# Kernel tuning notes

Measured on AMD Instinct MI355X. Metric: run time of the kernel, lower is better.

## Reference

```python
import jax, jax.numpy as jnp
import numpy as np

D_MODEL = 1024
D_STATE = 16
D_CONV = 4
EXPAND = 2
N_LAYERS = 4
D_INNER = EXPAND * D_MODEL          # 2048
DT_RANK = (D_MODEL + 15) // 16     # 64
BATCH, SEQ = 2, 1024
LN_EPS = 1e-5


def setup_inputs() -> dict:
    key = jax.random.key(0)
    ks = jax.random.split(key, 10)
    s = 0.02
    A_log = jnp.log(jnp.broadcast_to(
        jnp.arange(1, D_STATE + 1, dtype=jnp.float32), (N_LAYERS, D_INNER, D_STATE)))
    return {
        "x": jax.random.normal(ks[0], (BATCH, SEQ, D_MODEL), jnp.float32),
        "in_proj_w": jax.random.normal(ks[1], (N_LAYERS, 2 * D_INNER, D_MODEL), jnp.float32) * s,
        "conv_w": jax.random.normal(ks[2], (N_LAYERS, D_INNER, D_CONV), jnp.float32) * s,
        "conv_b": jnp.zeros((N_LAYERS, D_INNER), jnp.float32),
        "x_proj_w": jax.random.normal(ks[3], (N_LAYERS, DT_RANK + 2 * D_STATE, D_INNER), jnp.float32) * s,
        "dt_proj_w": jax.random.normal(ks[4], (N_LAYERS, D_INNER, DT_RANK), jnp.float32) * s,
        "dt_proj_b": jax.random.uniform(ks[5], (N_LAYERS, D_INNER), jnp.float32, -5.0, -3.0),
        "A_log": A_log,
        "D_skip": jnp.ones((N_LAYERS, D_INNER), jnp.float32),
        "out_proj_w": jax.random.normal(ks[6], (N_LAYERS, D_MODEL, D_INNER), jnp.float32) * s,
        "ln_g": jnp.ones((D_MODEL,), jnp.float32),
        "ln_b": jnp.zeros((D_MODEL,), jnp.float32),
    }


def _layer_norm(x, g, b):
    mu = jnp.mean(x, axis=-1, keepdims=True)
    var = jnp.mean(jnp.square(x - mu), axis=-1, keepdims=True)
    return (x - mu) * jax.lax.rsqrt(var + LN_EPS) * g + b


def _scan_combine(e1, e2):
    a1, b1 = e1
    a2, b2 = e2
    return a1 * a2, a2 * b1 + b2


def _mamba_block(x, in_w, cw, cb, xp_w, dt_w, dt_b, A_log, D_skip, out_w):
    # x: [B, L, D]
    xz = jnp.einsum('bld,ed->ble', x, in_w)          # [B, L, 2*d_inner]
    xm, z = jnp.split(xz, 2, axis=-1)
    # causal depthwise conv over time
    xc = jnp.transpose(xm, (0, 2, 1))                 # [B, d_inner, L]
    xc = jax.lax.conv_general_dilated(
        xc, cw[:, None, :], window_strides=(1,), padding=[(D_CONV - 1, 0)],
        feature_group_count=D_INNER, dimension_numbers=('NCH', 'OIH', 'NCH'))
    xm = jax.nn.silu(jnp.transpose(xc, (0, 2, 1)) + cb[None, None, :])
    # input-dependent dt, B, C
    xdbl = jnp.einsum('bld,ed->ble', xm, xp_w)        # [B, L, dt_rank + 2*S]
    dt, Bm, Cm = jnp.split(xdbl, [DT_RANK, DT_RANK + D_STATE], axis=-1)
    dt = jax.nn.softplus(jnp.einsum('blr,dr->bld', dt, dt_w) + dt_b)   # [B, L, d_inner]
    A = -jnp.exp(A_log)                               # [d_inner, S]
    dA = jnp.exp(dt[..., None] * A)                   # [B, L, d_inner, S]
    dBu = dt[..., None] * Bm[:, :, None, :] * xm[..., None]
    # selective scan: h_t = dA_t * h_{t-1} + dBu_t, via associative scan over L
    _, h = jax.lax.associative_scan(_scan_combine, (dA, dBu), axis=1)
    y = jnp.einsum('blds,bls->bld', h, Cm) + xm * D_skip
    y = y * jax.nn.silu(z)
    return jnp.einsum('bld,od->blo', y, out_w)        # [B, L, D]


def reference(x, in_proj_w, conv_w, conv_b, x_proj_w, dt_proj_w, dt_proj_b,
              A_log, D_skip, out_proj_w, ln_g, ln_b):
    for i in range(N_LAYERS):
        x = x + _mamba_block(_layer_norm(x, ln_g, ln_b),
                             in_proj_w[i], conv_w[i], conv_b[i], x_proj_w[i],
                             dt_proj_w[i], dt_proj_b[i], A_log[i], D_skip[i],
                             out_proj_w[i])
    return _layer_norm(x, ln_g, ln_b)
```

## Files before the change

kernel.cpp:

```cpp
#include <hip/hip_runtime.h>

#define NTOK 2048
#define SEQL 1024
#define DMODEL 1024
#define DINNER 2048
#define DSTATE 16
#define DTRANK 64
#define GCH 64
#define LC 16
#define XDS 128
#define XSPK 8

typedef __attribute__((ext_vector_type(8))) short short8;
typedef __attribute__((ext_vector_type(4))) float float4v;

__device__ __forceinline__ unsigned short f2bf(float f) {
    unsigned u = __float_as_uint(f);
    unsigned r = u + 0x7FFFu + ((u >> 16) & 1u);
    return (unsigned short)(r >> 16);
}
__device__ __forceinline__ float bf2f(unsigned short h) {
    return __uint_as_float(((unsigned)h) << 16);
}

__global__ __launch_bounds__(256) void f32_to_bf16_4(
    const float* __restrict__ s0, unsigned short* __restrict__ d0, int c0,
    const float* __restrict__ s1, unsigned short* __restrict__ d1, int c1,
    const float* __restrict__ s2, unsigned short* __restrict__ d2, int c2,
    const float* __restrict__ s3, unsigned short* __restrict__ d3, int c3) {
    int i = blockIdx.x * 256 + threadIdx.x;
    if (i >= c3) return;
    const float* s; unsigned short* dd; int j;
    if (i < c0)      { s = s0; dd = d0; j = i; }
    else if (i < c1) { s = s1; dd = d1; j = i - c0; }
    else if (i < c2) { s = s2; dd = d2; j = i - c1; }
    else             { s = s3; dd = d3; j = i - c2; }
    float4 a = ((const float4*)s)[4 * j];
    float4 b = ((const float4*)s)[4 * j + 1];
    float4 c = ((const float4*)s)[4 * j + 2];
    float4 d = ((const float4*)s)[4 * j + 3];
    uint4 v0, v1;
    v0.x = (unsigned)f2bf(a.x) | ((unsigned)f2bf(a.y) << 16);
    v0.y = (unsigned)f2bf(a.z) | ((unsigned)f2bf(a.w) << 16);
    v0.z = (unsigned)f2bf(b.x) | ((unsigned)f2bf(b.y) << 16);
    v0.w = (unsigned)f2bf(b.z) | ((unsigned)f2bf(b.w) << 16);
    v1.x = (unsigned)f2bf(c.x) | ((unsigned)f2bf(c.y) << 16);
    v1.y = (unsigned)f2bf(c.z) | ((unsigned)f2bf(c.w) << 16);
    v1.z = (unsigned)f2bf(d.x) | ((unsigned)f2bf(d.y) << 16);
    v1.w = (unsigned)f2bf(d.z) | ((unsigned)f2bf(d.w) << 16);
    ((uint4*)dd)[2 * j]     = v0;
    ((uint4*)dd)[2 * j + 1] = v1;
}

__global__ __launch_bounds__(256) void ln_kernel(
    const float* __restrict__ x, float* __restrict__ x_copy,
    const float* __restrict__ g, const float* __restrict__ b,
    unsigned short* __restrict__ out_bf) {
    int row = blockIdx.x;
    int t = threadIdx.x;
    float4 v = ((const float4*)(x + (size_t)row * DMODEL))[t];
    ((float4*)(x_copy + (size_t)row * DMODEL))[t] = v;
    float s  = v.x + v.y + v.z + v.w;
    float ss = v.x*v.x + v.y*v.y + v.z*v.z + v.w*v.w;
    for (int o = 32; o; o >>= 1) { s += __shfl_xor(s, o); ss += __shfl_xor(ss, o); }
    __shared__ float red[8];
    int wv = t >> 6;
    if ((t & 63) == 0) { red[wv * 2] = s; red[wv * 2 + 1] = ss; }
    __syncthreads();
    s  = red[0] + red[2] + red[4] + red[6];
    ss = red[1] + red[3] + red[5] + red[7];
    float mu = s * (1.f / DMODEL);
    float rstd = rsqrtf(ss * (1.f / DMODEL) - mu * mu + 1e-5f);
    float4 gv = ((const float4*)g)[t];
    float4 bv = ((const float4*)b)[t];
    ((ushort4*)out_bf)[row * 256 + t] = make_ushort4(
        f2bf((v.x - mu) * rstd * gv.x + bv.x),
        f2bf((v.y - mu) * rstd * gv.y + bv.y),
        f2bf((v.z - mu) * rstd * gv.z + bv.z),
        f2bf((v.w - mu) * rstd * gv.w + bv.w));
}

__global__ __launch_bounds__(256) void residual_ln(
    float* __restrict__ x_res, const float* __restrict__ p0,
    const float* __restrict__ p1, const float* __restrict__ p2,
    const float* __restrict__ p3, const float* __restrict__ g,
    const float* __restrict__ b, unsigned short* __restrict__ out_bf,
    float* __restrict__ out_f32) {
    int row = blockIdx.x;
    int t = threadIdx.x;
    size_t o4 = (size_t)row * 256 + t;
    float4 v  = ((const float4*)x_res)[o4];
    float4 a0 = ((const float4*)p0)[o4];
    float4 a1 = ((const float4*)p1)[o4];
    float4 a2 = ((const float4*)p2)[o4];
    float4 a3 = ((const float4*)p3)[o4];
    v.x += (a0.x + a1.x) + (a2.x + a3.x);
    v.y += (a0.y + a1.y) + (a2.y + a3.y);
    v.z += (a0.z + a1.z) + (a2.z + a3.z);
    v.w += (a0.w + a1.w) + (a2.w + a3.w);
    ((float4*)x_res)[o4] = v;
    float s  = v.x + v.y + v.z + v.w;
    float ss = v.x*v.x + v.y*v.y + v.z*v.z + v.w*v.w;
    for (int o = 32; o; o >>= 1) { s += __shfl_xor(s, o); ss += __shfl_xor(ss, o); }
    __shared__ float red[8];
    int wv = t >> 6;
    if ((t & 63) == 0) { red[wv * 2] = s; red[wv * 2 + 1] = ss; }
    __syncthreads();
    s  = red[0] + red[2] + red[4] + red[6];
    ss = red[1] + red[3] + red[5] + red[7];
    float mu = s * (1.f / DMODEL);
    float rstd = rsqrtf(ss * (1.f / DMODEL) - mu * mu + 1e-5f);
    float4 gv = ((const float4*)g)[t];
    float4 bv = ((const float4*)b)[t];
    float o0 = (v.x - mu) * rstd * gv.x + bv.x;
    float o1 = (v.y - mu) * rstd * gv.y + bv.y;
    float o2 = (v.z - mu) * rstd * gv.z + bv.z;
    float o3 = (v.w - mu) * rstd * gv.w + bv.w;
    if (out_f32) {
        ((float4*)out_f32)[o4] = make_float4(o0, o1, o2, o3);
    } else {
        ((ushort4*)out_bf)[o4] = make_ushort4(f2bf(o0), f2bf(o1), f2bf(o2), f2bf(o3));
    }
}

#define BKG 32
__global__ __launch_bounds__(256) void gemm64(
    const unsigned short* __restrict__ A, const unsigned short* __restrict__ B,
    void* __restrict__ Cv, const float* __restrict__ bias,
    int M, int N, int K, int Nb, int mode) {
    __shared__ __attribute__((aligned(16))) unsigned short As[3][128 * BKG];
    __shared__ __attribute__((aligned(16))) unsigned short Bs[3][64 * BKG];
    int m0 = blockIdx.y * 128, n0 = blockIdx.x * 64;
    int Klocal = K / gridDim.z;
    int kstart = blockIdx.z * Klocal;
    int t = threadIdx.x;
    int lane = t & 63, w = t >> 6;
    int tr = lane & 15, quad = lane >> 4;
    int r_l = lane >> 2;
    int q_l = (lane & 3) ^ ((lane >> 3) & 3);
    int col_l = q_l * 8;

    float4v acc[2][4];
    for (int mi = 0; mi < 2; ++mi)
        for (int ni = 0; ni < 4; ++ni)
            acc[mi][ni] = (float4v){0.f, 0.f, 0.f, 0.f};

    auto stage = [&](int kt, int buf) {
        int kbase = kstart + kt * BKG;
#pragma unroll
        for (int j = 0; j < 2; ++j) {
            int c = w * 2 + j;
            const unsigned short* ga = A + (size_t)(m0 + c * 16 + r_l) * K + kbase + col_l;
            __builtin_amdgcn_global_load_lds(
                (const __attribute__((address_space(1))) void*)ga,
                (__attribute__((address_space(3))) void*)(&As[buf][c * 512]),
                16, 0, 0);
        }
        int brow = n0 + w * 16 + r_l;
        if (brow >= Nb) brow = Nb - 1;
        const unsigned short* gb = B + (size_t)brow * K + kbase + col_l;
        __builtin_amdgcn_global_load_lds(
            (const __attribute__((address_space(1))) void*)gb,
            (__attribute__((address_space(3))) void*)(&Bs[buf][w * 512]),
            16, 0, 0);
    };

    int KT = Klocal / BKG;
    stage(0, 0);
    if (KT > 1) stage(1, 1);
    int u_off = (tr * 4 + (quad ^ ((tr >> 1) & 3))) * 8;
    for (int kt = 0; kt < KT; ++kt) {
        int cur = kt % 3;
        if (kt + 2 < KT) stage(kt + 2, (kt + 2) % 3);
        asm volatile("" ::: "memory");
        int nleft = KT - kt - 1;
        if (nleft >= 2)      __builtin_amdgcn_s_waitcnt(0x0F76);
        else if (nleft == 1) __builtin_amdgcn_s_waitcnt(0x0F73);
        else                 __builtin_amdgcn_s_waitcnt(0x0F70);
        __builtin_amdgcn_s_barrier();
        asm volatile("" ::: "memory");
        short8 af[2], bfr[4];
#pragma unroll
        for (int i = 0; i < 2; ++i)
            af[i] = *(const short8*)(&As[cur][(w * 2 + i) * 512 + u_off]);
#pragma unroll
        for (int i = 0; i < 4; ++i)
            bfr[i] = *(const short8*)(&Bs[cur][i * 512 + u_off]);
#pragma unroll
        for (int mi = 0; mi < 2; ++mi)
#pragma unroll
            for (int ni = 0; ni < 4; ++ni)
                acc[mi][ni] = __builtin_amdgcn_mfma_f32_16x16x32_bf16(
                    af[mi], bfr[ni], acc[mi][ni], 0, 0, 0);
        asm volatile("" ::: "memory");
        __builtin_amdgcn_s_barrier();
        asm volatile("" ::: "memory");
    }
    size_t zoff = (size_t)blockIdx.z * M * N;
    for (int mi = 0; mi < 2; ++mi)
        for (int ni = 0; ni < 4; ++ni) {
            int col = n0 + ni * 16 + tr;
            int rowb = m0 + w * 32 + mi * 16 + quad * 4;
            for (int r = 0; r < 4; ++r) {
                size_t off = (size_t)(rowb + r) * N + col;
                float val = acc[mi][ni][r];
                if (mode == 0) {
                    ((float*)Cv)[zoff + off] = val;
                } else if (mode == 2) {
                    ((unsigned short*)Cv)[off] = f2bf(val);
                } else {
                    float v2 = val + bias[col];
                    float sp = (v2 > 15.f) ? v2 : log1pf(expf(v2));
                    ((unsigned short*)Cv)[off] = f2bf(sp);
                }
            }
        }
}

__global__ __launch_bounds__(256) void reduce_xp(
    const float* __restrict__ part, unsigned short* __restrict__ dtA,
    float* __restrict__ BC) {
    int i = blockIdx.x * 256 + threadIdx.x;
    int row = i >> 7, col = i & 127;
    float s = 0.f;
#pragma unroll
    for (int z = 0; z < XSPK; ++z)
        s += part[(size_t)z * NTOK * XDS + i];
    if (col < 64) dtA[row * 64 + col] = f2bf(s);
    else if (col < 96) BC[row * 32 + (col - 64)] = s;
}

__global__ __launch_bounds__(256) void conv_silu(
    const unsigned short* __restrict__ xz, const float* __restrict__ cw,
    const float* __restrict__ cb, unsigned short* __restrict__ xm_bf) {
    int i = blockIdx.x * 256 + threadIdx.x;
    int c8 = i & (DINNER / 8 - 1);
    int tk = i >> 8;
    int l = tk & (SEQL - 1);
    int c = c8 * 8;
    const unsigned short* base = xz + (size_t)tk * (2 * DINNER) + c;
    short8 r3 = {0,0,0,0,0,0,0,0}, r2 = {0,0,0,0,0,0,0,0}, r1 = {0,0,0,0,0,0,0,0};
    if (l >= 3) r3 = *(const short8*)(base - 3 * 2 * DINNER);
    if (l >= 2) r2 = *(const short8*)(base - 2 * 2 * DINNER);
    if (l >= 1) r1 = *(const short8*)(base - 1 * 2 * DINNER);
    short8 r0 = *(const short8*)(base);
    short8 out;
#pragma unroll
    for (int j = 0; j < 8; ++j) {
        float4 wv = ((const float4*)cw)[c + j];
        float acc = cb[c + j]
            + bf2f((unsigned short)r3[j]) * wv.x
            + bf2f((unsigned short)r2[j]) * wv.y
            + bf2f((unsigned short)r1[j]) * wv.z
            + bf2f((unsigned short)r0[j]) * wv.w;
        float sv = acc / (1.f + expf(-acc));
        out[j] = (short)f2bf(sv);
    }
    *(short8*)(xm_bf + (size_t)tk * DINNER + c) = out;
}

__global__ __launch_bounds__(256) void scan_a(
    const unsigned short* __restrict__ dt_bf, const unsigned short* __restrict__ xm_bf,
    const float* __restrict__ BC, const float* __restrict__ A_log,
    float* __restrict__ h_end, float* __restrict__ S_chunk) {
    int bid = blockIdx.x;
    int g = bid >> 4, b = (bid >> 3) & 1, cbk = bid & 7;
    int c = cbk * 256 + threadIdx.x;
    __shared__ float Bsh[LC][16];
    {
        int li = threadIdx.x >> 4, s = threadIdx.x & 15;
        Bsh[li][s] = BC[((size_t)(b * SEQL + g * LC + li)) * 32 + s];
    }
    __syncthreads();
    float a_l2[16], h[16];
#pragma unroll
    for (int s = 0; s < 16; ++s) {
        a_l2[s] = -expf(A_log[c * 16 + s]) * 1.44269504f;
        h[s] = 0.f;
    }
    float S = 0.f;
    int rowbase = b * SEQL + g * LC;
    for (int i = 0; i < LC; ++i) {
        size_t off = (size_t)(rowbase + i) * DINNER + c;
        float dtv = bf2f(dt_bf[off]);
        S += dtv;
        float u = bf2f(xm_bf[off]);
        float bu = dtv * u;
#pragma unroll
        for (int s = 0; s < 16; ++s) {
            float dA = exp2f(dtv * a_l2[s]);
            h[s] = dA * h[s] + Bsh[i][s] * bu;
        }
    }
    int gb = g * 2 + b;
#pragma unroll
    for (int s = 0; s < 16; ++s)
        h_end[((size_t)gb * 16 + s) * DINNER + c] = h[s];
    S_chunk[(size_t)gb * DINNER + c] = S;
}

__global__ __launch_bounds__(256) void scan_b(
    const float* __restrict__ A_log, const float* __restrict__ S_chunk,
    const float* __restrict__ h_end, float* __restrict__ h_in) {
    int idx = blockIdx.x * 256 + threadIdx.x;
    int c = idx & (DINNER - 1);
    int s = (idx >> 11) & 15;
    int b = idx >> 15;
    float a_l2 = -expf(A_log[c * 16 + s]) * 1.44269504f;
    float h = 0.f;
    for (int g = 0; g < GCH; ++g) {
        int gb = g * 2 + b;
        h_in[((size_t)gb * 16 + s) * DINNER + c] = h;
        float P = exp2f(a_l2 * S_chunk[(size_t)gb * DINNER + c]);
        h = P * h + h_end[((size_t)gb * 16 + s) * DINNER + c];
    }
}

__global__ __launch_bounds__(256) void scan_c(
    const unsigned short* __restrict__ dt_bf, const unsigned short* __restrict__ xm_bf,
    const float* __restrict__ BC, const float* __restrict__ A_log,
    const float* __restrict__ D_skip, const unsigned short* __restrict__ xz,
    const float* __restrict__ h_in, unsigned short* __restrict__ y_bf) {
    int bid = blockIdx.x;
    int g = bid >> 4, b = (bid >> 3) & 1, cbk = bid & 7;
    int c = cbk * 256 + threadIdx.x;
    __shared__ float BCsh[LC][32];
    for (int r = 0; r < 2; ++r) {
        int e = threadIdx.x + r * 256;
        int li = e >> 5, s = e & 31;
        BCsh[li][s] = BC[((size_t)(b * SEQL + g * LC + li)) * 32 + s];
    }
    __syncthreads();
    int gb = g * 2 + b;
    float a_l2[16], h[16];
#pragma unroll
    for (int s = 0; s < 16; ++s) {
        a_l2[s] = -expf(A_log[c * 16 + s]) * 1.44269504f;
        h[s] = h_in[((size_t)gb * 16 + s) * DINNER + c];
    }
    float dsk = D_skip[c];
    int rowbase = b * SEQL + g * LC;
    for (int i = 0; i < LC; ++i) {
        size_t off = (size_t)(rowbase + i) * DINNER + c;
        float dtv = bf2f(dt_bf[off]);
        float u = bf2f(xm_bf[off]);
        float bu = dtv * u;
        float y = 0.f;
#pragma unroll
        for (int s = 0; s < 16; ++s) {
            float dA = exp2f(dtv * a_l2[s]);
            h[s] = dA * h[s] + BCsh[i][s] * bu;
            y += h[s] * BCsh[i][16 + s];
        }
        y += u * dsk;
        float zv = bf2f(xz[(size_t)(rowbase + i) * (2 * DINNER) + DINNER + c]);
        y *= zv / (1.f + expf(-zv));
        y_bf[off] = f2bf(y);
    }
}

extern "C" void kernel_launch(void* const* d_in, const int* in_sizes, int n_in,
                              void* d_out, int out_size, void* d_ws, size_t ws_size,
                              hipStream_t stream) {
    const float* x_in   = (const float*)d_in[0];
    const float* in_w   = (const float*)d_in[1];
    const float* conv_w = (const float*)d_in[2];
    const float* conv_b = (const float*)d_in[3];
    const float* xp_w   = (const float*)d_in[4];
    const float* dt_w   = (const float*)d_in[5];
    const float* dt_b   = (const float*)d_in[6];
    const float* A_logp = (const float*)d_in[7];
    const float* Dsk    = (const float*)d_in[8];
    const float* out_w  = (const float*)d_in[9];
    const float* ln_g   = (const float*)d_in[10];
    const float* ln_b   = (const float*)d_in[11];
    float* outp = (float*)d_out;

    char* p = (char*)d_ws;
    auto alloc = [&](size_t bytes) {
        void* r = (void*)p;
        p += (bytes + 255) & ~(size_t)255;
        return r;
    };
    float* x_res  = (float*)alloc((size_t)NTOK * DMODEL * 4);
    unsigned short* xn_bf = (unsigned short*)alloc((size_t)NTOK * DMODEL * 2);
    unsigned short* xz_bf = (unsigned short*)alloc((size_t)NTOK * 2 * DINNER * 2);
    unsigned short* xm_bf = (unsigned short*)alloc((size_t)NTOK * DINNER * 2);
    float* xp_part = (float*)alloc((size_t)XSPK * NTOK * XDS * 4);
    float* out_part = (float*)alloc((size_t)4 * NTOK * DMODEL * 4);
    float* BC     = (float*)alloc((size_t)NTOK * 32 * 4);
    unsigned short* dtA_bf = (unsigned short*)alloc((size_t)NTOK * DTRANK * 2);
    unsigned short* dt_bf = (unsigned short*)alloc((size_t)NTOK * DINNER * 2);
    unsigned short* y_bf = (unsigned short*)alloc((size_t)NTOK * DINNER * 2);
    float* h_end  = (float*)alloc((size_t)GCH * 2 * 16 * DINNER * 4);
    float* h_in   = (float*)alloc((size_t)GCH * 2 * 16 * DINNER * 4);
    float* S_chunk = (float*)alloc((size_t)GCH * 2 * DINNER * 4);
    int n_inw  = 4 * 2 * DINNER * DMODEL;
    int n_xpw  = 4 * 96 * DINNER;
    int n_dtw  = 4 * DINNER * DTRANK;
    int n_outw = 4 * DMODEL * DINNER;
    unsigned short* wbf_in  = (unsigned short*)alloc((size_t)n_inw * 2);
    unsigned short* wbf_xp  = (unsigned short*)alloc((size_t)n_xpw * 2);
    unsigned short* wbf_dt  = (unsigned short*)alloc((size_t)n_dtw * 2);
    unsigned short* wbf_out = (unsigned short*)alloc((size_t)n_outw * 2);

    int c0 = n_inw / 16;
    int c1 = c0 + n_xpw / 16;
    int c2 = c1 + n_dtw / 16;
    int c3 = c2 + n_outw / 16;
    f32_to_bf16_4<<<(c3 + 255) / 256, 256, 0, stream>>>(
        in_w, wbf_in, c0, xp_w, wbf_xp, c1, dt_w, wbf_dt, c2, out_w, wbf_out, c3);

    ln_kernel<<<NTOK, 256, 0, stream>>>(x_in, x_res, ln_g, ln_b, xn_bf);

    for (int L = 0; L < 4; ++L) {
        const unsigned short* w_in  = wbf_in  + (size_t)L * 2 * DINNER * DMODEL;
        const float*          w_cv  = conv_w  + (size_t)L * DINNER * 4;
        const float*          b_cv  = conv_b  + (size_t)L * DINNER;
        const unsigned short* w_xp  = wbf_xp  + (size_t)L * 96 * DINNER;
        const unsigned short* w_dt  = wbf_dt  + (size_t)L * DINNER * DTRANK;
        const float*          b_dt  = dt_b    + (size_t)L * DINNER;
        const float*          al    = A_logp  + (size_t)L * DINNER * DSTATE;
        const float*          dskl  = Dsk     + (size_t)L * DINNER;
        const unsigned short* w_out = wbf_out + (size_t)L * DMODEL * DINNER;

        gemm64<<<dim3(64, 16, 1), 256, 0, stream>>>(
            xn_bf, w_in, xz_bf, nullptr, NTOK, 2 * DINNER, DMODEL, 2 * DINNER, 2);
        conv_silu<<<NTOK * (DINNER / 8) / 256, 256, 0, stream>>>(xz_bf, w_cv, b_cv, xm_bf);
        gemm64<<<dim3(2, 16, XSPK), 256, 0, stream>>>(
            xm_bf, w_xp, xp_part, nullptr, NTOK, XDS, DINNER, 96, 0);
        reduce_xp<<<NTOK * XDS / 256, 256, 0, stream>>>(xp_part, dtA_bf, BC);
        gemm64<<<dim3(32, 16, 1), 256, 0, stream>>>(
            dtA_bf, w_dt, dt_bf, b_dt, NTOK, DINNER, DTRANK, DINNER, 3);
        scan_a<<<GCH * 16, 256, 0, stream>>>(dt_bf, xm_bf, BC, al, h_end, S_chunk);
        scan_b<<<2 * 16 * DINNER / 256, 256, 0, stream>>>(al, S_chunk, h_end, h_in);
        scan_c<<<GCH * 16, 256, 0, stream>>>(dt_bf, xm_bf, BC, al, dskl, xz_bf,
                                             h_in, y_bf);
        gemm64<<<dim3(16, 16, 4), 256, 0, stream>>>(
            y_bf, w_out, out_part, nullptr, NTOK, DMODEL, DINNER, DMODEL, 0);
        residual_ln<<<NTOK, 256, 0, stream>>>(
            x_res, out_part, out_part + (size_t)NTOK * DMODEL,
            out_part + (size_t)2 * NTOK * DMODEL, out_part + (size_t)3 * NTOK * DMODEL,
            ln_g, ln_b, (L < 3) ? xn_bf : nullptr, (L < 3) ? nullptr : outp);
    }
}
```

Before: 876.2 us.

## Fuse three scan kernels into one persistent kernel with grid barriers

Merges scan_a, scan_b and scan_c into a single kernel that uses a global atomic-counter grid barrier between the phases. Registers holding a_l2 and the shared BC tile are reused across phases, and two kernel launches plus their reloads are removed. The 1024-block grid must be fully co-resident (launch_bounds 256,4 on 256 CUs) or the barrier deadlocks. The counter is reset in the weight-conversion kernel and offset per layer.

```diff
diff --git a/kernel.cpp b/kernel.cpp
--- a/kernel.cpp
+++ b/kernel.cpp
@@ -23,12 +23,26 @@
     return __uint_as_float(((unsigned)h) << 16);
 }
 
+__device__ __forceinline__ void grid_bar(unsigned* cnt, unsigned target) {
+    __syncthreads();
+    if (threadIdx.x == 0) {
+        __threadfence();
+        atomicAdd(cnt, 1u);
+        while (__hip_atomic_load(cnt, __ATOMIC_ACQUIRE, __HIP_MEMORY_SCOPE_AGENT)
+               < target)
+            __builtin_amdgcn_s_sleep(8);
+    }
+    __syncthreads();
+}
+
 __global__ __launch_bounds__(256) void f32_to_bf16_4(
     const float* __restrict__ s0, unsigned short* __restrict__ d0, int c0,
     const float* __restrict__ s1, unsigned short* __restrict__ d1, int c1,
     const float* __restrict__ s2, unsigned short* __restrict__ d2, int c2,
-    const float* __restrict__ s3, unsigned short* __restrict__ d3, int c3) {
+    const float* __restrict__ s3, unsigned short* __restrict__ d3, int c3,
+    unsigned* __restrict__ bar) {
     int i = blockIdx.x * 256 + threadIdx.x;
+    if (i == 0) *bar = 0u;
     if (i >= c3) return;
     const float* s; unsigned short* dd; int j;
     if (i < c0)      { s = s0; dd = d0; j = i; }
@@ -259,17 +273,21 @@
     *(short8*)(xm_bf + (size_t)tk * DINNER + c) = out;
 }
 
-__global__ __launch_bounds__(256) void scan_a(
+__global__ __launch_bounds__(256, 4) void scan_fused(
     const unsigned short* __restrict__ dt_bf, const unsigned short* __restrict__ xm_bf,
     const float* __restrict__ BC, const float* __restrict__ A_log,
-    float* __restrict__ h_end, float* __restrict__ S_chunk) {
+    const float* __restrict__ D_skip, const unsigned short* __restrict__ xz,
+    float* __restrict__ h_end, float* __restrict__ S_chunk,
+    float* __restrict__ h_in, unsigned short* __restrict__ y_bf,
+    unsigned* __restrict__ bar, unsigned tbase) {
     int bid = blockIdx.x;
     int g = bid >> 4, b = (bid >> 3) & 1, cbk = bid & 7;
     int c = cbk * 256 + threadIdx.x;
-    __shared__ float Bsh[LC][16];
-    {
-        int li = threadIdx.x >> 4, s = threadIdx.x & 15;
-        Bsh[li][s] = BC[((size_t)(b * SEQL + g * LC + li)) * 32 + s];
+    __shared__ float BCsh[LC][32];
+    for (int r = 0; r < 2; ++r) {
+        int e = threadIdx.x + r * 256;
+        int li = e >> 5, s = e & 31;
+        BCsh[li][s] = BC[((size_t)(b * SEQL + g * LC + li)) * 32 + s];
     }
     __syncthreads();
     float a_l2[16], h[16];
@@ -289,7 +307,7 @@
 #pragma unroll
         for (int s = 0; s < 16; ++s) {
             float dA = exp2f(dtv * a_l2[s]);
-            h[s] = dA * h[s] + Bsh[i][s] * bu;
+            h[s] = dA * h[s] + BCsh[i][s] * bu;
         }
     }
     int gb = g * 2 + b;
@@ -297,49 +315,30 @@
     for (int s = 0; s < 16; ++s)
         h_end[((size_t)gb * 16 + s) * DINNER + c] = h[s];
     S_chunk[(size_t)gb * DINNER + c] = S;
-}
-
-__global__ __launch_bounds__(256) void scan_b(
-    const float* __restrict__ A_log, const float* __restrict__ S_chunk,
-    const float* __restrict__ h_end, float* __restrict__ h_in) {
-    int idx = blockIdx.x * 256 + threadIdx.x;
-    int c = idx & (DINNER - 1);
-    int s = (idx >> 11) & 15;
-    int b = idx >> 15;
-    float a_l2 = -expf(A_log[c * 16 + s]) * 1.44269504f;
-    float h = 0.f;
-    for (int g = 0; g < GCH; ++g) {
-        int gb = g * 2 + b;
-        h_in[((size_t)gb * 16 + s) * DINNER + c] = h;
-        float P = exp2f(a_l2 * S_chunk[(size_t)gb * DINNER + c]);
-        h = P * h + h_end[((size_t)gb * 16 + s) * DINNER + c];
-    }
-}
-
-__global__ __launch_bounds__(256) void scan_c(
-    const unsigned short* __restrict__ dt_bf, const unsigned short* __restrict__ xm_bf,
-    const float* __restrict__ BC, const float* __restrict__ A_log,
-    const float* __restrict__ D_skip, const unsigned short* __restrict__ xz,
-    const float* __restrict__ h_in, unsigned short* __restrict__ y_bf) {
-    int bid = blockIdx.x;
-    int g = bid >> 4, b = (bid >> 3) & 1, cbk = bid & 7;
-    int c = cbk * 256 + threadIdx.x;
-    __shared__ float BCsh[LC][32];
-    for (int r = 0; r < 2; ++r) {
-        int e = threadIdx.x + r * 256;
-        int li = e >> 5, s = e & 31;
-        BCsh[li][s] = BC[((size_t)(b * SEQL + g * LC + li)) * 32 + s];
-    }
-    __syncthreads();
-    int gb = g * 2 + b;
-    float a_l2[16], h[16];
-#pragma unroll
-    for (int s = 0; s < 16; ++s) {
-        a_l2[s] = -expf(A_log[c * 16 + s]) * 1.44269504f;
+
+    grid_bar(bar, tbase + 1024);
+
+    if (bid < 256) {
+        int idx = bid * 256 + threadIdx.x;
+        int cc = idx & (DINNER - 1);
+        int ss = (idx >> 11) & 15;
+        int bb = idx >> 15;
+        float al2 = -expf(A_log[cc * 16 + ss]) * 1.44269504f;
+        float hh = 0.f;
+        for (int gg = 0; gg < GCH; ++gg) {
+            int gb2 = gg * 2 + bb;
+            h_in[((size_t)gb2 * 16 + ss) * DINNER + cc] = hh;
+            float P = exp2f(al2 * S_chunk[(size_t)gb2 * DINNER + cc]);
+            hh = P * hh + h_end[((size_t)gb2 * 16 + ss) * DINNER + cc];
+        }
+    }
+
+    grid_bar(bar, tbase + 2048);
+
+#pragma unroll
+    for (int s = 0; s < 16; ++s)
         h[s] = h_in[((size_t)gb * 16 + s) * DINNER + c];
-    }
     float dsk = D_skip[c];
-    int rowbase = b * SEQL + g * LC;
     for (int i = 0; i < LC; ++i) {
         size_t off = (size_t)(rowbase + i) * DINNER + c;
         float dtv = bf2f(dt_bf[off]);
@@ -395,6 +394,7 @@
     float* h_end  = (float*)alloc((size_t)GCH * 2 * 16 * DINNER * 4);
     float* h_in   = (float*)alloc((size_t)GCH * 2 * 16 * DINNER * 4);
     float* S_chunk = (float*)alloc((size_t)GCH * 2 * DINNER * 4);
+    unsigned* bar = (unsigned*)alloc(256);
     int n_inw  = 4 * 2 * DINNER * DMODEL;
     int n_xpw  = 4 * 96 * DINNER;
     int n_dtw  = 4 * DINNER * DTRANK;
@@ -409,7 +409,7 @@
     int c2 = c1 + n_dtw / 16;
     int c3 = c2 + n_outw / 16;
     f32_to_bf16_4<<<(c3 + 255) / 256, 256, 0, stream>>>(
-        in_w, wbf_in, c0, xp_w, wbf_xp, c1, dt_w, wbf_dt, c2, out_w, wbf_out, c3);
+        in_w, wbf_in, c0, xp_w, wbf_xp, c1, dt_w, wbf_dt, c2, out_w, wbf_out, c3, bar);
 
     ln_kernel<<<NTOK, 256, 0, stream>>>(x_in, x_res, ln_g, ln_b, xn_bf);
 
@@ -432,10 +432,9 @@
         reduce_xp<<<NTOK * XDS / 256, 256, 0, stream>>>(xp_part, dtA_bf, BC);
         gemm64<<<dim3(32, 16, 1), 256, 0, stream>>>(
             dtA_bf, w_dt, dt_bf, b_dt, NTOK, DINNER, DTRANK, DINNER, 3);
-        scan_a<<<GCH * 16, 256, 0, stream>>>(dt_bf, xm_bf, BC, al, h_end, S_chunk);
-        scan_b<<<2 * 16 * DINNER / 256, 256, 0, stream>>>(al, S_chunk, h_end, h_in);
-        scan_c<<<GCH * 16, 256, 0, stream>>>(dt_bf, xm_bf, BC, al, dskl, xz_bf,
-                                             h_in, y_bf);
+        scan_fused<<<GCH * 16, 256, 0, stream>>>(
+            dt_bf, xm_bf, BC, al, dskl, xz_bf, h_end, S_chunk, h_in, y_bf,
+            bar, (unsigned)(L * 2048));
         gemm64<<<dim3(16, 16, 4), 256, 0, stream>>>(
             y_bf, w_out, out_part, nullptr, NTOK, DMODEL, DINNER, DMODEL, 0);
         residual_ln<<<NTOK, 256, 0, stream>>>(
```

After: 2.516 ms. 187% more time.

## Fuse dt projection and softplus into scan kernels, drop dt GEMM

Applied to the files above, without the earlier changes.

Removes the separate dt_proj GEMM and its bf16 dt buffer. Each scan kernel now recomputes dt per channel from the low-rank dtA vectors in shared memory and a transposed, pair-packed dt weight held in registers, then applies softplus inline. This avoids writing and reading a token-by-d_inner dt tensor and saves one launch per layer. In exchange the dt dot products are done twice (scan_a and scan_c) with scalar FMAs, and the kernels use 32 more registers each. A new kernel transposes the dt weights once at setup.

```diff
diff --git a/kernel.cpp b/kernel.cpp
--- a/kernel.cpp
+++ b/kernel.cpp
@@ -22,19 +22,19 @@
 __device__ __forceinline__ float bf2f(unsigned short h) {
     return __uint_as_float(((unsigned)h) << 16);
 }
-
-__global__ __launch_bounds__(256) void f32_to_bf16_4(
+__device__ __forceinline__ float bflo(unsigned u) { return __uint_as_float(u << 16); }
+__device__ __forceinline__ float bfhi(unsigned u) { return __uint_as_float(u & 0xffff0000u); }
+
+__global__ __launch_bounds__(256) void f32_to_bf16_3(
     const float* __restrict__ s0, unsigned short* __restrict__ d0, int c0,
     const float* __restrict__ s1, unsigned short* __restrict__ d1, int c1,
-    const float* __restrict__ s2, unsigned short* __restrict__ d2, int c2,
-    const float* __restrict__ s3, unsigned short* __restrict__ d3, int c3) {
+    const float* __restrict__ s2, unsigned short* __restrict__ d2, int c2) {
     int i = blockIdx.x * 256 + threadIdx.x;
-    if (i >= c3) return;
+    if (i >= c2) return;
     const float* s; unsigned short* dd; int j;
     if (i < c0)      { s = s0; dd = d0; j = i; }
     else if (i < c1) { s = s1; dd = d1; j = i - c0; }
-    else if (i < c2) { s = s2; dd = d2; j = i - c1; }
-    else             { s = s3; dd = d3; j = i - c2; }
+    else             { s = s2; dd = d2; j = i - c1; }
     float4 a = ((const float4*)s)[4 * j];
     float4 b = ((const float4*)s)[4 * j + 1];
     float4 c = ((const float4*)s)[4 * j + 2];
@@ -50,6 +50,17 @@
     v1.w = (unsigned)f2bf(d.z) | ((unsigned)f2bf(d.w) << 16);
     ((uint4*)dd)[2 * j]     = v0;
     ((uint4*)dd)[2 * j + 1] = v1;
+}
+
+__global__ __launch_bounds__(256) void cvt_dtT(
+    const float* __restrict__ w, unsigned short* __restrict__ wT) {
+    int idx = blockIdx.x * 256 + threadIdx.x;
+    int c = idx & (DINNER - 1);
+    int r = (idx >> 11) & 63;
+    int l = idx >> 17;
+    size_t lbase = (size_t)l * 64 * DINNER;
+    wT[lbase + ((size_t)(r >> 1) * DINNER + c) * 2 + (r & 1)] =
+        f2bf(w[(size_t)l * DINNER * 64 + (size_t)c * 64 + r]);
 }
 
 __global__ __launch_bounds__(256) void ln_kernel(
@@ -126,8 +137,7 @@
 #define BKG 32
 __global__ __launch_bounds__(256) void gemm64(
     const unsigned short* __restrict__ A, const unsigned short* __restrict__ B,
-    void* __restrict__ Cv, const float* __restrict__ bias,
-    int M, int N, int K, int Nb, int mode) {
+    void* __restrict__ Cv, int M, int N, int K, int Nb, int mode) {
     __shared__ __attribute__((aligned(16))) unsigned short As[3][128 * BKG];
     __shared__ __attribute__((aligned(16))) unsigned short Bs[3][64 * BKG];
     int m0 = blockIdx.y * 128, n0 = blockIdx.x * 64;
@@ -206,12 +216,8 @@
                 float val = acc[mi][ni][r];
                 if (mode == 0) {
                     ((float*)Cv)[zoff + off] = val;
-                } else if (mode == 2) {
+                } else {
                     ((unsigned short*)Cv)[off] = f2bf(val);
-                } else {
-                    float v2 = val + bias[col];
-                    float sp = (v2 > 15.f) ? v2 : log1pf(expf(v2));
-                    ((unsigned short*)Cv)[off] = f2bf(sp);
                 }
             }
         }
@@ -260,18 +266,28 @@
 }
 
 __global__ __launch_bounds__(256) void scan_a(
-    const unsigned short* __restrict__ dt_bf, const unsigned short* __restrict__ xm_bf,
+    const unsigned short* __restrict__ dtA, const unsigned short* __restrict__ wdtT,
+    const float* __restrict__ dtb, const unsigned short* __restrict__ xm_bf,
     const float* __restrict__ BC, const float* __restrict__ A_log,
     float* __restrict__ h_end, float* __restrict__ S_chunk) {
     int bid = blockIdx.x;
     int g = bid >> 4, b = (bid >> 3) & 1, cbk = bid & 7;
     int c = cbk * 256 + threadIdx.x;
+    int rowbase = b * SEQL + g * LC;
     __shared__ float Bsh[LC][16];
+    __shared__ unsigned dtash[LC * 32];
     {
         int li = threadIdx.x >> 4, s = threadIdx.x & 15;
-        Bsh[li][s] = BC[((size_t)(b * SEQL + g * LC + li)) * 32 + s];
+        Bsh[li][s] = BC[((size_t)(rowbase + li)) * 32 + s];
+        ((uint2*)dtash)[threadIdx.x] =
+            ((const uint2*)(dtA + (size_t)rowbase * 64))[threadIdx.x];
     }
     __syncthreads();
+    unsigned wp[32];
+#pragma unroll
+    for (int r2 = 0; r2 < 32; ++r2)
+        wp[r2] = ((const unsigned*)wdtT)[(size_t)r2 * DINNER + c];
+    float dbias = dtb[c];
     float a_l2[16], h[16];
 #pragma unroll
     for (int s = 0; s < 16; ++s) {
@@ -279,11 +295,16 @@
         h[s] = 0.f;
     }
     float S = 0.f;
-    int rowbase = b * SEQL + g * LC;
     for (int i = 0; i < LC; ++i) {
+        float acc = dbias;
+#pragma unroll
+        for (int r2 = 0; r2 < 32; ++r2) {
+            unsigned dv = dtash[i * 32 + r2];
+            acc += bflo(dv) * bflo(wp[r2]) + bfhi(dv) * bfhi(wp[r2]);
+        }
+        float dtv = (acc > 15.f) ? acc : log1pf(expf(acc));
+        S += dtv;
         size_t off = (size_t)(rowbase + i) * DINNER + c;
-        float dtv = bf2f(dt_bf[off]);
-        S += dtv;
         float u = bf2f(xm_bf[off]);
         float bu = dtv * u;
 #pragma unroll
@@ -317,20 +338,30 @@
 }
 
 __global__ __launch_bounds__(256) void scan_c(
-    const unsigned short* __restrict__ dt_bf, const unsigned short* __restrict__ xm_bf,
+    const unsigned short* __restrict__ dtA, const unsigned short* __restrict__ wdtT,
+    const float* __restrict__ dtb, const unsigned short* __restrict__ xm_bf,
     const float* __restrict__ BC, const float* __restrict__ A_log,
     const float* __restrict__ D_skip, const unsigned short* __restrict__ xz,
     const float* __restrict__ h_in, unsigned short* __restrict__ y_bf) {
     int bid = blockIdx.x;
     int g = bid >> 4, b = (bid >> 3) & 1, cbk = bid & 7;
     int c = cbk * 256 + threadIdx.x;
+    int rowbase = b * SEQL + g * LC;
     __shared__ float BCsh[LC][32];
+    __shared__ unsigned dtash[LC * 32];
     for (int r = 0; r < 2; ++r) {
         int e = threadIdx.x + r * 256;
         int li = e >> 5, s = e & 31;
-        BCsh[li][s] = BC[((size_t)(b * SEQL + g * LC + li)) * 32 + s];
-    }
+        BCsh[li][s] = BC[((size_t)(rowbase + li)) * 32 + s];
+    }
+    ((uint2*)dtash)[threadIdx.x] =
+        ((const uint2*)(dtA + (size_t)rowbase * 64))[threadIdx.x];
     __syncthreads();
+    unsigned wp[32];
+#pragma unroll
+    for (int r2 = 0; r2 < 32; ++r2)
+        wp[r2] = ((const unsigned*)wdtT)[(size_t)r2 * DINNER + c];
+    float dbias = dtb[c];
     int gb = g * 2 + b;
     float a_l2[16], h[16];
 #pragma unroll
@@ -339,10 +370,15 @@
         h[s] = h_in[((size_t)gb * 16 + s) * DINNER + c];
     }
     float dsk = D_skip[c];
-    int rowbase = b * SEQL + g * LC;
     for (int i = 0; i < LC; ++i) {
+        float acc = dbias;
+#pragma unroll
+        for (int r2 = 0; r2 < 32; ++r2) {
+            unsigned dv = dtash[i * 32 + r2];
+            acc += bflo(dv) * bflo(wp[r2]) + bfhi(dv) * bfhi(wp[r2]);
+        }
+        float dtv = (acc > 15.f) ? acc : log1pf(expf(acc));
         size_t off = (size_t)(rowbase + i) * DINNER + c;
-        float dtv = bf2f(dt_bf[off]);
         float u = bf2f(xm_bf[off]);
         float bu = dtv * u;
         float y = 0.f;
@@ -390,7 +426,6 @@
     float* out_part = (float*)alloc((size_t)4 * NTOK * DMODEL * 4);
     float* BC     = (float*)alloc((size_t)NTOK * 32 * 4);
     unsigned short* dtA_bf = (unsigned short*)alloc((size_t)NTOK * DTRANK * 2);
-    unsigned short* dt_bf = (unsigned short*)alloc((size_t)NTOK * DINNER * 2);
     unsigned short* y_bf = (unsigned short*)alloc((size_t)NTOK * DINNER * 2);
     float* h_end  = (float*)alloc((size_t)GCH * 2 * 16 * DINNER * 4);
     float* h_in   = (float*)alloc((size_t)GCH * 2 * 16 * DINNER * 4);
@@ -401,15 +436,15 @@
     int n_outw = 4 * DMODEL * DINNER;
     unsigned short* wbf_in  = (unsigned short*)alloc((size_t)n_inw * 2);
     unsigned short* wbf_xp  = (unsigned short*)alloc((size_t)n_xpw * 2);
-    unsigned short* wbf_dt  = (unsigned short*)alloc((size_t)n_dtw * 2);
+    unsigned short* wbf_dtT = (unsigned short*)alloc((size_t)n_dtw * 2);
     unsigned short* wbf_out = (unsigned short*)alloc((size_t)n_outw * 2);
 
     int c0 = n_inw / 16;
     int c1 = c0 + n_xpw / 16;
-    int c2 = c1 + n_dtw / 16;
-    int c3 = c2 + n_outw / 16;
-    f32_to_bf16_4<<<(c3 + 255) / 256, 256, 0, stream>>>(
-        in_w, wbf_in, c0, xp_w, wbf_xp, c1, dt_w, wbf_dt, c2, out_w, wbf_out, c3);
+    int c2 = c1 + n_outw / 16;
+    f32_to_bf16_3<<<(c2 + 255) / 256, 256, 0, stream>>>(
+        in_w, wbf_in, c0, xp_w, wbf_xp, c1, out_w, wbf_out, c2);
+    cvt_dtT<<<n_dtw / 256, 256, 0, stream>>>(dt_w, wbf_dtT);
 
     ln_kernel<<<NTOK, 256, 0, stream>>>(x_in, x_res, ln_g, ln_b, xn_bf);
 
@@ -418,26 +453,25 @@
         const float*          w_cv  = conv_w  + (size_t)L * DINNER * 4;
         const float*          b_cv  = conv_b  + (size_t)L * DINNER;
         const unsigned short* w_xp  = wbf_xp  + (size_t)L * 96 * DINNER;
-        const unsigned short* w_dt  = wbf_dt  + (size_t)L * DINNER * DTRANK;
+        const unsigned short* w_dtT = wbf_dtT + (size_t)L * 64 * DINNER;
         const float*          b_dt  = dt_b    + (size_t)L * DINNER;
         const float*          al    = A_logp  + (size_t)L * DINNER * DSTATE;
         const float*          dskl  = Dsk     + (size_t)L * DINNER;
         const unsigned short* w_out = wbf_out + (size_t)L * DMODEL * DINNER;
 
         gemm64<<<dim3(64, 16, 1), 256, 0, stream>>>(
-            xn_bf, w_in, xz_bf, nullptr, NTOK, 2 * DINNER, DMODEL, 2 * DINNER, 2);
+            xn_bf, w_in, xz_bf, NTOK, 2 * DINNER, DMODEL, 2 * DINNER, 2);
         conv_silu<<<NTOK * (DINNER / 8) / 256, 256, 0, stream>>>(xz_bf, w_cv, b_cv, xm_bf);
         gemm64<<<dim3(2, 16, XSPK), 256, 0, stream>>>(
-            xm_bf, w_xp, xp_part, nullptr, NTOK, XDS, DINNER, 96, 0);
+            xm_bf, w_xp, xp_part, NTOK, XDS, DINNER, 96, 0);
         reduce_xp<<<NTOK * XDS / 256, 256, 0, stream>>>(xp_part, dtA_bf, BC);
-        gemm64<<<dim3(32, 16, 1), 256, 0, stream>>>(
-            dtA_bf, w_dt, dt_bf, b_dt, NTOK, DINNER, DTRANK, DINNER, 3);
-        scan_a<<<GCH * 16, 256, 0, stream>>>(dt_bf, xm_bf, BC, al, h_end, S_chunk);
+        scan_a<<<GCH * 16, 256, 0, stream>>>(dtA_bf, w_dtT, b_dt, xm_bf, BC, al,
+                                             h_end, S_chunk);
         scan_b<<<2 * 16 * DINNER / 256, 256, 0, stream>>>(al, S_chunk, h_end, h_in);
-        scan_c<<<GCH * 16, 256, 0, stream>>>(dt_bf, xm_bf, BC, al, dskl, xz_bf,
-                                             h_in, y_bf);
+        scan_c<<<GCH * 16, 256, 0, stream>>>(dtA_bf, w_dtT, b_dt, xm_bf, BC, al,
+                                             dskl, xz_bf, h_in, y_bf);
         gemm64<<<dim3(16, 16, 4), 256, 0, stream>>>(
-            y_bf, w_out, out_part, nullptr, NTOK, DMODEL, DINNER, DMODEL, 0);
+            y_bf, w_out, out_part, NTOK, DMODEL, DINNER, DMODEL, 0);
         residual_ln<<<NTOK, 256, 0, stream>>>(
             x_res, out_part, out_part + (size_t)NTOK * DMODEL,
             out_part + (size_t)2 * NTOK * DMODEL, out_part + (size_t)3 * NTOK * DMODEL,
```

New measurement: 962.1 us. 9.8% more time.

## Fuse dt_proj GEMM and softplus into scan kernels, drop dt buffer

Applied to the files above, without the earlier changes.

Removes the separate dt_proj GEMM launch and the NTOK x DINNER bf16 dt buffer. Each scan_a and scan_c block now computes its 16x256 dt tile with MFMA from the low-rank dtA and dt_proj weights, applies bias and softplus, and keeps the result in LDS. This saves a kernel launch plus the global write and two reads of dt per layer. In exchange the dt GEMM and softplus are computed twice, once in each scan kernel, and the scan kernels use more LDS.

```diff
diff --git a/kernel.cpp b/kernel.cpp
--- a/kernel.cpp
+++ b/kernel.cpp
@@ -126,8 +126,7 @@
 #define BKG 32
 __global__ __launch_bounds__(256) void gemm64(
     const unsigned short* __restrict__ A, const unsigned short* __restrict__ B,
-    void* __restrict__ Cv, const float* __restrict__ bias,
-    int M, int N, int K, int Nb, int mode) {
+    void* __restrict__ Cv, int M, int N, int K, int Nb, int mode) {
     __shared__ __attribute__((aligned(16))) unsigned short As[3][128 * BKG];
     __shared__ __attribute__((aligned(16))) unsigned short Bs[3][64 * BKG];
     int m0 = blockIdx.y * 128, n0 = blockIdx.x * 64;
@@ -206,12 +205,8 @@
                 float val = acc[mi][ni][r];
                 if (mode == 0) {
                     ((float*)Cv)[zoff + off] = val;
-                } else if (mode == 2) {
+                } else {
                     ((unsigned short*)Cv)[off] = f2bf(val);
-                } else {
-                    float v2 = val + bias[col];
-                    float sp = (v2 > 15.f) ? v2 : log1pf(expf(v2));
-                    ((unsigned short*)Cv)[off] = f2bf(sp);
                 }
             }
         }
@@ -260,16 +255,47 @@
 }
 
 __global__ __launch_bounds__(256) void scan_a(
-    const unsigned short* __restrict__ dt_bf, const unsigned short* __restrict__ xm_bf,
+    const unsigned short* __restrict__ dtA, const unsigned short* __restrict__ wdt,
+    const float* __restrict__ dtb, const unsigned short* __restrict__ xm_bf,
     const float* __restrict__ BC, const float* __restrict__ A_log,
     float* __restrict__ h_end, float* __restrict__ S_chunk) {
     int bid = blockIdx.x;
     int g = bid >> 4, b = (bid >> 3) & 1, cbk = bid & 7;
-    int c = cbk * 256 + threadIdx.x;
+    int tid = threadIdx.x;
+    int c0 = cbk * 256;
+    int c = c0 + tid;
+    int rowbase = b * SEQL + g * LC;
     __shared__ float Bsh[LC][16];
+    __shared__ __attribute__((aligned(16))) unsigned short dtash[LC * 64];
+    __shared__ unsigned short dt_lds[LC * 256];
     {
-        int li = threadIdx.x >> 4, s = threadIdx.x & 15;
-        Bsh[li][s] = BC[((size_t)(b * SEQL + g * LC + li)) * 32 + s];
+        int li = tid >> 4, s = tid & 15;
+        Bsh[li][s] = BC[((size_t)(rowbase + li)) * 32 + s];
+        ((uint2*)dtash)[tid] = ((const uint2*)(dtA + (size_t)rowbase * 64))[tid];
+    }
+    __syncthreads();
+    {
+        int lane = tid & 63, wn = tid >> 6;
+        int l15 = lane & 15, quad = lane >> 4;
+        short8 a0 = *(const short8*)(dtash + l15 * 64 + quad * 8);
+        short8 a1 = *(const short8*)(dtash + l15 * 64 + 32 + quad * 8);
+#pragma unroll
+        for (int nt = 0; nt < 4; ++nt) {
+            int ch = wn * 64 + nt * 16 + l15;
+            const unsigned short* wrow = wdt + (size_t)(c0 + ch) * 64;
+            short8 b0 = *(const short8*)(wrow + quad * 8);
+            short8 b1 = *(const short8*)(wrow + 32 + quad * 8);
+            float4v acc = (float4v){0.f, 0.f, 0.f, 0.f};
+            acc = __builtin_amdgcn_mfma_f32_16x16x32_bf16(a0, b0, acc, 0, 0, 0);
+            acc = __builtin_amdgcn_mfma_f32_16x16x32_bf16(a1, b1, acc, 0, 0, 0);
+            float bias = dtb[c0 + ch];
+#pragma unroll
+            for (int r = 0; r < 4; ++r) {
+                float v2 = acc[r] + bias;
+                float sp = (v2 > 15.f) ? v2 : log1pf(expf(v2));
+                dt_lds[(quad * 4 + r) * 256 + ch] = f2bf(sp);
+            }
+        }
     }
     __syncthreads();
     float a_l2[16], h[16];
@@ -279,12 +305,10 @@
         h[s] = 0.f;
     }
     float S = 0.f;
-    int rowbase = b * SEQL + g * LC;
     for (int i = 0; i < LC; ++i) {
-        size_t off = (size_t)(rowbase + i) * DINNER + c;
-        float dtv = bf2f(dt_bf[off]);
+        float dtv = bf2f(dt_lds[i * 256 + tid]);
         S += dtv;
-        float u = bf2f(xm_bf[off]);
+        float u = bf2f(xm_bf[(size_t)(rowbase + i) * DINNER + c]);
         float bu = dtv * u;
 #pragma unroll
         for (int s = 0; s < 16; ++s) {
@@ -317,18 +341,49 @@
 }
 
 __global__ __launch_bounds__(256) void scan_c(
-    const unsigned short* __restrict__ dt_bf, const unsigned short* __restrict__ xm_bf,
+    const unsigned short* __restrict__ dtA, const unsigned short* __restrict__ wdt,
+    const float* __restrict__ dtb, const unsigned short* __restrict__ xm_bf,
     const float* __restrict__ BC, const float* __restrict__ A_log,
     const float* __restrict__ D_skip, const unsigned short* __restrict__ xz,
     const float* __restrict__ h_in, unsigned short* __restrict__ y_bf) {
     int bid = blockIdx.x;
     int g = bid >> 4, b = (bid >> 3) & 1, cbk = bid & 7;
-    int c = cbk * 256 + threadIdx.x;
+    int tid = threadIdx.x;
+    int c0 = cbk * 256;
+    int c = c0 + tid;
+    int rowbase = b * SEQL + g * LC;
     __shared__ float BCsh[LC][32];
+    __shared__ __attribute__((aligned(16))) unsigned short dtash[LC * 64];
+    __shared__ unsigned short dt_lds[LC * 256];
     for (int r = 0; r < 2; ++r) {
-        int e = threadIdx.x + r * 256;
+        int e = tid + r * 256;
         int li = e >> 5, s = e & 31;
-        BCsh[li][s] = BC[((size_t)(b * SEQL + g * LC + li)) * 32 + s];
+        BCsh[li][s] = BC[((size_t)(rowbase + li)) * 32 + s];
+    }
+    ((uint2*)dtash)[tid] = ((const uint2*)(dtA + (size_t)rowbase * 64))[tid];
+    __syncthreads();
+    {
+        int lane = tid & 63, wn = tid >> 6;
+        int l15 = lane & 15, quad = lane >> 4;
+        short8 a0 = *(const short8*)(dtash + l15 * 64 + quad * 8);
+        short8 a1 = *(const short8*)(dtash + l15 * 64 + 32 + quad * 8);
+#pragma unroll
+        for (int nt = 0; nt < 4; ++nt) {
+            int ch = wn * 64 + nt * 16 + l15;
+            const unsigned short* wrow = wdt + (size_t)(c0 + ch) * 64;
+            short8 b0 = *(const short8*)(wrow + quad * 8);
+            short8 b1 = *(const short8*)(wrow + 32 + quad * 8);
+            float4v acc = (float4v){0.f, 0.f, 0.f, 0.f};
+            acc = __builtin_amdgcn_mfma_f32_16x16x32_bf16(a0, b0, acc, 0, 0, 0);
+            acc = __builtin_amdgcn_mfma_f32_16x16x32_bf16(a1, b1, acc, 0, 0, 0);
+            float bias = dtb[c0 + ch];
+#pragma unroll
+            for (int r = 0; r < 4; ++r) {
+                float v2 = acc[r] + bias;
+                float sp = (v2 > 15.f) ? v2 : log1pf(expf(v2));
+                dt_lds[(quad * 4 + r) * 256 + ch] = f2bf(sp);
+            }
+        }
     }
     __syncthreads();
     int gb = g * 2 + b;
@@ -339,10 +394,9 @@
         h[s] = h_in[((size_t)gb * 16 + s) * DINNER + c];
     }
     float dsk = D_skip[c];
-    int rowbase = b * SEQL + g * LC;
     for (int i = 0; i < LC; ++i) {
         size_t off = (size_t)(rowbase + i) * DINNER + c;
-        float dtv = bf2f(dt_bf[off]);
+        float dtv = bf2f(dt_lds[i * 256 + tid]);
         float u = bf2f(xm_bf[off]);
         float bu = dtv * u;
         float y = 0.f;
@@ -390,7 +444,6 @@
     float* out_part = (float*)alloc((size_t)4 * NTOK * DMODEL * 4);
     float* BC     = (float*)alloc((size_t)NTOK * 32 * 4);
     unsigned short* dtA_bf = (unsigned short*)alloc((size_t)NTOK * DTRANK * 2);
-    unsigned short* dt_bf = (unsigned short*)alloc((size_t)NTOK * DINNER * 2);
     unsigned short* y_bf = (unsigned short*)alloc((size_t)NTOK * DINNER * 2);
     float* h_end  = (float*)alloc((size_t)GCH * 2 * 16 * DINNER * 4);
     float* h_in   = (float*)alloc((size_t)GCH * 2 * 16 * DINNER * 4);
@@ -425,19 +478,18 @@
         const unsigned short* w_out = wbf_out + (size_t)L * DMODEL * DINNER;
 
         gemm64<<<dim3(64, 16, 1), 256, 0, stream>>>(
-            xn_bf, w_in, xz_bf, nullptr, NTOK, 2 * DINNER, DMODEL, 2 * DINNER, 2);
+            xn_bf, w_in, xz_bf, NTOK, 2 * DINNER, DMODEL, 2 * DINNER, 2);
         conv_silu<<<NTOK * (DINNER / 8) / 256, 256, 0, stream>>>(xz_bf, w_cv, b_cv, xm_bf);
         gemm64<<<dim3(2, 16, XSPK), 256, 0, stream>>>(
-            xm_bf, w_xp, xp_part, nullptr, NTOK, XDS, DINNER, 96, 0);
+            xm_bf, w_xp, xp_part, NTOK, XDS, DINNER, 96, 0);
         reduce_xp<<<NTOK * XDS / 256, 256, 0, stream>>>(xp_part, dtA_bf, BC);
-        gemm64<<<dim3(32, 16, 1), 256, 0, stream>>>(
-            dtA_bf, w_dt, dt_bf, b_dt, NTOK, DINNER, DTRANK, DINNER, 3);
-        scan_a<<<GCH * 16, 256, 0, stream>>>(dt_bf, xm_bf, BC, al, h_end, S_chunk);
+        scan_a<<<GCH * 16, 256, 0, stream>>>(dtA_bf, w_dt, b_dt, xm_bf, BC, al,
+                                             h_end, S_chunk);
         scan_b<<<2 * 16 * DINNER / 256, 256, 0, stream>>>(al, S_chunk, h_end, h_in);
-        scan_c<<<GCH * 16, 256, 0, stream>>>(dt_bf, xm_bf, BC, al, dskl, xz_bf,
-                                             h_in, y_bf);
+        scan_c<<<GCH * 16, 256, 0, stream>>>(dtA_bf, w_dt, b_dt, xm_bf, BC, al,
+                                             dskl, xz_bf, h_in, y_bf);
         gemm64<<<dim3(16, 16, 4), 256, 0, stream>>>(
-            y_bf, w_out, out_part, nullptr, NTOK, DMODEL, DINNER, DMODEL, 0);
+            y_bf, w_out, out_part, NTOK, DMODEL, DINNER, DMODEL, 0);
         residual_ln<<<NTOK, 256, 0, stream>>>(
             x_res, out_part, out_part + (size_t)NTOK * DMODEL,
             out_part + (size_t)2 * NTOK * DMODEL, out_part + (size_t)3 * NTOK * DMODEL,
```

New measurement: 870.8 us. Within noise of the previous version (-0.6%).
